# Optimization experiments

Measured on AMD Instinct MI355X. Metric: run time of the kernel, lower is better.

The kernel has to match this reference:

```python
import jax, jax.numpy as jnp
import numpy as np
from jax import lax

B, T, F = 32, 2048, 512
K, D = 1024, 512
CAL = 8
G_MIN, G_MAX = 0.05, 0.75
EPS = 1e-5  # torch LayerNorm default


def setup_inputs() -> dict:
    key = jax.random.key(0)
    ks = jax.random.split(key, 3)
    x = jax.random.normal(ks[0], (B, T, F), dtype=jnp.float32)
    # kaiming_normal_ (fan_in mode, relu gain sqrt(2)) on Linear weights, zero bias
    P_w = jax.random.normal(ks[1], (K, F), dtype=jnp.float32) * np.sqrt(2.0 / F)
    W_w = jax.random.normal(ks[2], (D, K), dtype=jnp.float32) * np.sqrt(2.0 / K)
    return {
        "x": x,
        "P_w": P_w,
        "W_w": W_w,
        "W_b": jnp.zeros((D,), jnp.float32),
        "b": jnp.zeros((D,), jnp.float32),
        "ln_g": jnp.ones((D,), jnp.float32),
        "ln_b": jnp.zeros((D,), jnp.float32),
        "alpha": jnp.float32(0.0),
        "theta1": jnp.float32(0.2),
        "phi1": jnp.float32(0.1),
        "theta2": jnp.float32(0.3),
        "phi2": jnp.float32(0.05),
        "w1": jnp.float32(1.0),
        "w2": jnp.float32(1.0),
        "b_g": jnp.float32(0.0),
    }


def reference(x, P_w, W_w, W_b, b, ln_g, ln_b, alpha, theta1, phi1, theta2, phi2, w1, w2, b_g):
    # --- gate: <Z> of RX(phi) RY(theta) |0> == cos(theta) * cos(phi) ---
    z1 = jnp.cos(theta1) * jnp.cos(phi1)
    z2 = jnp.cos(theta2) * jnp.cos(phi2)
    g = jnp.clip(jax.nn.sigmoid(w1 * z1 + w2 * z2 + b_g), G_MIN, G_MAX)

    # --- calibration scalar (F >= CAL branch) ---
    cal_scalar = x[..., -CAL:].mean(axis=1).mean(axis=1)  # [B]

    # --- per-step linear + bias + alpha*cal, vectorized over (B, T) ---
    proj = jnp.einsum("btf,kf->btk", x, P_w)                    # [B,T,K]
    base = jnp.einsum("btk,dk->btd", proj, W_w) + W_b + b        # [B,T,D]
    base = base + alpha * cal_scalar[:, None, None]

    # --- LayerNorm over last dim (biased variance, as torch) ---
    mu = base.mean(axis=-1, keepdims=True)
    var = jnp.mean(jnp.square(base - mu), axis=-1, keepdims=True)
    base = (base - mu) * lax.rsqrt(var + EPS) * ln_g + ln_b      # [B,T,D]

    # --- scalar-gate EMA recurrence: h_t = (1-g) h_{t-1} + g * base_t ---
    def step(h, bt):
        h = (1.0 - g) * h + g * bt
        return h, None

    h0 = jnp.zeros((x.shape[0], D), dtype=base.dtype)
    h, _ = lax.scan(step, h0, jnp.moveaxis(base, 1, 0))          # scan over T
    return h
```

## Files before the change

### kernel.cpp

```cpp
#include <hip/hip_runtime.h>

#define BB   32
#define TT   2048
#define FF   512
#define KK   1024
#define DD   512
#define NCMAX 512
#define LN_EPS 1e-5f
#define WCUT 1e-12f

typedef __attribute__((ext_vector_type(8))) short bf16x8;
typedef __attribute__((ext_vector_type(4))) float f32x4;

__device__ __forceinline__ float compute_g(const float* th1, const float* ph1,
                                           const float* th2, const float* ph2,
                                           const float* w1, const float* w2,
                                           const float* bg) {
    float z1 = cosf(*th1) * cosf(*ph1);
    float z2 = cosf(*th2) * cosf(*ph2);
    float s  = (*w1) * z1 + (*w2) * z2 + (*bg);
    float sg = 1.0f / (1.0f + expf(-s));
    return fminf(fmaxf(sg, 0.05f), 0.75f);
}

__device__ __forceinline__ ushort f2bf(float x) {
    unsigned u = __float_as_uint(x);
    u += 0x7FFFu + ((u >> 16) & 1u);
    return (ushort)(u >> 16);
}

__global__ __launch_bounds__(256) void weight_merge(
    const float* __restrict__ Pw, const float* __restrict__ Ww,
    ushort* __restrict__ Cbf, float* __restrict__ wj, int* __restrict__ nact,
    float* __restrict__ out,
    const float* th1, const float* ph1, const float* th2, const float* ph2,
    const float* w1p, const float* w2p, const float* bgp) {

    __shared__ __align__(16) ushort As[32 * 16 * 8];
    __shared__ __align__(16) ushort Bs[32 * 16 * 8];
    __shared__ int cnt4[4];

    const int tid = threadIdx.x;

    if (blockIdx.x == 0) {
        const float g   = compute_g(th1, ph1, th2, ph2, w1p, w2p, bgp);
        const float omg = 1.0f - g;
        const float w0  = g * powf(omg, (float)tid);
        const float w1  = g * powf(omg, (float)(tid + 256));
        wj[tid]       = w0;
        wj[tid + 256] = w1;
        const unsigned long long m0 = __ballot(w0 >= WCUT);
        const unsigned long long m1 = __ballot(w1 >= WCUT);
        if ((tid & 63) == 0) cnt4[tid >> 6] = __popcll(m0) + __popcll(m1);
        __syncthreads();
        if (tid == 0) *nact = cnt4[0] + cnt4[1] + cnt4[2] + cnt4[3];
    } else if (blockIdx.x == 1) {
        float4 z = make_float4(0.f, 0.f, 0.f, 0.f);
        #pragma unroll
        for (int i = 0; i < BB * DD / 4 / 256; ++i)
            *(float4*)(out + (size_t)(i * 256 + tid) * 4) = z;
    }

    const int d0 = (blockIdx.x >> 4) * 32;
    const int f0 = (blockIdx.x & 15) * 32;

    const int wave = tid >> 6;
    const int lane = tid & 63;
    const int wm2  = wave >> 1;
    const int wn2  = wave & 1;
    const int lg   = lane >> 4;
    const int ll   = lane & 15;

    const int srow = tid & 31;
    const int so   = tid >> 5;

    const int arow = wm2 * 16 + ll;
    const int brow = wn2 * 16 + ll;

    f32x4 accA = {0.f, 0.f, 0.f, 0.f};
    f32x4 accB = {0.f, 0.f, 0.f, 0.f};

    float a0[8], a1[8], b0[8], b1[8];

#define WM_LOAD(kkv) do {                                                         \
        const float* wr = Ww + (size_t)(d0 + srow) * KK + (kkv);                  \
        *(float4*)&a0[0] = *(const float4*)(wr + so * 8);                         \
        *(float4*)&a0[4] = *(const float4*)(wr + so * 8 + 4);                     \
        *(float4*)&a1[0] = *(const float4*)(wr + (so + 8) * 8);                   \
        *(float4*)&a1[4] = *(const float4*)(wr + (so + 8) * 8 + 4);               \
        const float* pr = Pw + (size_t)(kkv) * FF + f0 + srow;                    \
        _Pragma("unroll")                                                         \
        for (int j = 0; j < 8; ++j) {                                             \
            b0[j] = pr[(size_t)(so * 8 + j) * FF];                                \
            b1[j] = pr[(size_t)((so + 8) * 8 + j) * FF];                          \
        }                                                                         \
    } while (0)

#define WM_STORE() do {                                                           \
        bf16x8 va0, va1, vb0, vb1;                                                \
        _Pragma("unroll")                                                         \
        for (int e = 0; e < 8; ++e) {                                             \
            va0[e] = (short)f2bf(a0[e]); va1[e] = (short)f2bf(a1[e]);             \
            vb0[e] = (short)f2bf(b0[e]); vb1[e] = (short)f2bf(b1[e]);             \
        }                                                                         \
        const int sw = srow & 15;                                                 \
        *(bf16x8*)&As[(srow * 16 + (so ^ sw)) * 8]       = va0;                   \
        *(bf16x8*)&As[(srow * 16 + ((so + 8) ^ sw)) * 8] = va1;                   \
        *(bf16x8*)&Bs[(srow * 16 + (so ^ sw)) * 8]       = vb0;                   \
        *(bf16x8*)&Bs[(srow * 16 + ((so + 8) ^ sw)) * 8] = vb1;                   \
    } while (0)

    WM_LOAD(0);

    for (int kk = 0; kk < KK; kk += 128) {
        WM_STORE();
        __syncthreads();
        if (kk + 128 < KK) WM_LOAD(kk + 128);

        #pragma unroll
        for (int ks = 0; ks < 4; ++ks) {
            const int oct = ks * 4 + lg;
            const bf16x8 af = *(const bf16x8*)&As[(arow * 16 + (oct ^ (arow & 15))) * 8];
            const bf16x8 bf = *(const bf16x8*)&Bs[(brow * 16 + (oct ^ (brow & 15))) * 8];
            if (ks & 1) accB = __builtin_amdgcn_mfma_f32_16x16x32_bf16(af, bf, accB, 0, 0, 0);
            else        accA = __builtin_amdgcn_mfma_f32_16x16x32_bf16(af, bf, accA, 0, 0, 0);
        }
        __syncthreads();
    }
#undef WM_LOAD
#undef WM_STORE

    {
        const f32x4 acc = accA + accB;
        const int fb = f0 + wn2 * 16 + ll;
        const int db = d0 + wm2 * 16 + lg * 4;
        ushort* cp = Cbf + ((size_t)(fb >> 3) * DD) * 8 + (fb & 7);
        #pragma unroll
        for (int j = 0; j < 4; ++j)
            cp[(size_t)(db + j) * 8] = f2bf(acc[j]);
    }
}

__global__ __launch_bounds__(512) void base_ln(
    const float* __restrict__ x, const ushort* __restrict__ Cbf,
    const float* __restrict__ Wb, const float* __restrict__ bvec,
    const float* __restrict__ lng, const float* __restrict__ lnb,
    const float* __restrict__ wj, const int* __restrict__ nact,
    float* __restrict__ out) {

    const int nv = *nact;
    const int cslot = blockIdx.x;
    if (cslot >= nv) return;
    const int rh = blockIdx.y;

    __shared__ __align__(16) ushort xls[16 * 64 * 8];
    __shared__ float redw[8][4][4][2];

    const int tid  = threadIdx.x;
    const int w    = tid >> 6;
    const int lane = tid & 63;
    const int ll   = lane & 15;
    const int lg   = lane >> 4;

    float bias[4], gam[4], bet[4];
    #pragma unroll
    for (int j = 0; j < 4; ++j) {
        const int d = w * 64 + j * 16 + ll;
        bias[j] = Wb[d] + bvec[d];
        gam[j]  = lng[d];
        bet[j]  = lnb[d];
    }

    float hacc[4][4];
    #pragma unroll
    for (int j = 0; j < 4; ++j)
        #pragma unroll
        for (int r = 0; r < 4; ++r) hacc[j][r] = 0.f;

    for (int c = cslot; c < nv; c += 64) {
        const int t = TT - 1 - c;

        #pragma unroll
        for (int i2 = 0; i2 < 2; ++i2) {
            const int i = tid + i2 * 512;
            const int r = i >> 6, o = i & 63;
            const float* src = x + ((size_t)(rh * 16 + r) * TT + t) * FF + o * 8;
            const float4 u0 = *(const float4*)src;
            const float4 u1 = *(const float4*)(src + 4);
            bf16x8 v;
            v[0] = (short)f2bf(u0.x); v[1] = (short)f2bf(u0.y);
            v[2] = (short)f2bf(u0.z); v[3] = (short)f2bf(u0.w);
            v[4] = (short)f2bf(u1.x); v[5] = (short)f2bf(u1.y);
            v[6] = (short)f2bf(u1.z); v[7] = (short)f2bf(u1.w);
            *(bf16x8*)&xls[(r * 64 + (o ^ (r & 7))) * 8] = v;
        }
        __syncthreads();

        f32x4 acc0 = {0.f,0.f,0.f,0.f}, acc1 = {0.f,0.f,0.f,0.f};
        f32x4 acc2 = {0.f,0.f,0.f,0.f}, acc3 = {0.f,0.f,0.f,0.f};

        #pragma unroll 4
        for (int ks = 0; ks < 16; ++ks) {
            const int oct = ks * 4 + lg;
            const bf16x8 af = *(const bf16x8*)&xls[(ll * 64 + (oct ^ (ll & 7))) * 8];
            const ushort* cp = Cbf + ((size_t)oct * DD + w * 64 + ll) * 8;
            const bf16x8 bf0 = *(const bf16x8*)(cp);
            const bf16x8 bf1 = *(const bf16x8*)(cp + 16 * 8);
            const bf16x8 bf2 = *(const bf16x8*)(cp + 32 * 8);
            const bf16x8 bf3 = *(const bf16x8*)(cp + 48 * 8);
            acc0 = __builtin_amdgcn_mfma_f32_16x16x32_bf16(af, bf0, acc0, 0, 0, 0);
            acc1 = __builtin_amdgcn_mfma_f32_16x16x32_bf16(af, bf1, acc1, 0, 0, 0);
            acc2 = __builtin_amdgcn_mfma_f32_16x16x32_bf16(af, bf2, acc2, 0, 0, 0);
            acc3 = __builtin_amdgcn_mfma_f32_16x16x32_bf16(af, bf3, acc3, 0, 0, 0);
        }

        float v[4][4];
        #pragma unroll
        for (int r = 0; r < 4; ++r) {
            v[0][r] = acc0[r] + bias[0];
            v[1][r] = acc1[r] + bias[1];
            v[2][r] = acc2[r] + bias[2];
            v[3][r] = acc3[r] + bias[3];
        }

        float S[4], Q[4];
        #pragma unroll
        for (int r = 0; r < 4; ++r) {
            S[r] = v[0][r] + v[1][r] + v[2][r] + v[3][r];
            Q[r] = v[0][r]*v[0][r] + v[1][r]*v[1][r] + v[2][r]*v[2][r] + v[3][r]*v[3][r];
        }
        #pragma unroll
        for (int off = 8; off >= 1; off >>= 1) {
            #pragma unroll
            for (int r = 0; r < 4; ++r) {
                S[r] += __shfl_xor(S[r], off);
                Q[r] += __shfl_xor(Q[r], off);
            }
        }
        if (ll == 0) {
            #pragma unroll
            for (int r = 0; r < 4; ++r) {
                redw[w][lg][r][0] = S[r];
                redw[w][lg][r][1] = Q[r];
            }
        }
        __syncthreads();

        const float wjc = wj[c];
        #pragma unroll
        for (int r = 0; r < 4; ++r) {
            float SS = 0.f, QQ = 0.f;
            #pragma unroll
            for (int q = 0; q < 8; ++q) {
                SS += redw[q][lg][r][0];
                QQ += redw[q][lg][r][1];
            }
            const float mu   = SS * (1.0f / DD);
            const float rstd = rsqrtf(QQ * (1.0f / DD) - mu * mu + LN_EPS);
            #pragma unroll
            for (int j = 0; j < 4; ++j)
                hacc[j][r] += wjc * ((v[j][r] - mu) * rstd * gam[j] + bet[j]);
        }
        __syncthreads();
    }

    #pragma unroll
    for (int r = 0; r < 4; ++r) {
        const int row = rh * 16 + lg * 4 + r;
        #pragma unroll
        for (int j = 0; j < 4; ++j)
            atomicAdd(out + (size_t)row * DD + w * 64 + j * 16 + ll, hacc[j][r]);
    }
}

extern "C" void kernel_launch(void* const* d_in, const int* in_sizes, int n_in,
                              void* d_out, int out_size, void* d_ws, size_t ws_size,
                              hipStream_t stream) {
    const float* x   = (const float*)d_in[0];
    const float* Pw  = (const float*)d_in[1];
    const float* Ww  = (const float*)d_in[2];
    const float* Wb  = (const float*)d_in[3];
    const float* bv  = (const float*)d_in[4];
    const float* lng = (const float*)d_in[5];
    const float* lnb = (const float*)d_in[6];
    const float* th1 = (const float*)d_in[8];
    const float* ph1 = (const float*)d_in[9];
    const float* th2 = (const float*)d_in[10];
    const float* ph2 = (const float*)d_in[11];
    const float* w1  = (const float*)d_in[12];
    const float* w2  = (const float*)d_in[13];
    const float* bg  = (const float*)d_in[14];

    ushort* Cbf  = (ushort*)d_ws;
    float*  wj   = (float*)((char*)d_ws + (1 << 19));
    int*    nact = (int*)(wj + 512);

    weight_merge<<<256, 256, 0, stream>>>(Pw, Ww, Cbf, wj, nact, (float*)d_out,
                                          th1, ph1, th2, ph2, w1, w2, bg);

    dim3 bgrid(64, 2);
    base_ln<<<bgrid, 512, 0, stream>>>(x, Cbf, Wb, bv, lng, lnb, wj, nact,
                                       (float*)d_out);
}
```

Baseline: 25.94 us.

## Double-buffer weight-merge GEMM staging and coalesce W_w row loads

The weight-merge kernel that forms W_w·P_w now keeps two LDS buffers and two register stages, prefetching two K-tiles ahead, and drops one of the two barriers per iteration. W_w loads are remapped so eight threads read contiguous float4s along a row (rwq/kq8), which coalesces better than the previous per-row pattern. This is meant to hide global load latency in a small prologue GEMM. In exchange it doubles LDS and register use for staging.

Result: faster. 23.18 us (-10.7%).

```diff
diff --git a/kernel.cpp b/kernel.cpp
--- a/kernel.cpp
+++ b/kernel.cpp
@@ -36,8 +36,8 @@
     const float* th1, const float* ph1, const float* th2, const float* ph2,
     const float* w1p, const float* w2p, const float* bgp) {
 
-    __shared__ __align__(16) ushort As[32 * 16 * 8];
-    __shared__ __align__(16) ushort Bs[32 * 16 * 8];
+    __shared__ __align__(16) ushort As[2][32 * 16 * 8];
+    __shared__ __align__(16) ushort Bs[2][32 * 16 * 8];
     __shared__ int cnt4[4];
 
     const int tid = threadIdx.x;
@@ -71,6 +71,8 @@
     const int lg   = lane >> 4;
     const int ll   = lane & 15;
 
+    const int rwq = tid >> 3;
+    const int kq8 = tid & 7;
     const int srow = tid & 31;
     const int so   = tid >> 5;
 
@@ -80,52 +82,60 @@
     f32x4 accA = {0.f, 0.f, 0.f, 0.f};
     f32x4 accB = {0.f, 0.f, 0.f, 0.f};
 
-    float a0[8], a1[8], b0[8], b1[8];
-
-#define WM_LOAD(kkv) do {                                                         \
-        const float* wr = Ww + (size_t)(d0 + srow) * KK + (kkv);                  \
-        *(float4*)&a0[0] = *(const float4*)(wr + so * 8);                         \
-        *(float4*)&a0[4] = *(const float4*)(wr + so * 8 + 4);                     \
-        *(float4*)&a1[0] = *(const float4*)(wr + (so + 8) * 8);                   \
-        *(float4*)&a1[4] = *(const float4*)(wr + (so + 8) * 8 + 4);               \
+    float4 aw[2][4];
+    float  pb0[2][8], pb1[2][8];
+
+#define WM_LOAD(S, kkv) do {                                                      \
+        const float* wr = Ww + (size_t)(d0 + rwq) * KK + (kkv) + kq8 * 4;         \
+        _Pragma("unroll")                                                         \
+        for (int it = 0; it < 4; ++it)                                            \
+            aw[S][it] = *(const float4*)(wr + it * 32);                           \
         const float* pr = Pw + (size_t)(kkv) * FF + f0 + srow;                    \
         _Pragma("unroll")                                                         \
         for (int j = 0; j < 8; ++j) {                                             \
-            b0[j] = pr[(size_t)(so * 8 + j) * FF];                                \
-            b1[j] = pr[(size_t)((so + 8) * 8 + j) * FF];                          \
+            pb0[S][j] = pr[(size_t)(so * 8 + j) * FF];                            \
+            pb1[S][j] = pr[(size_t)((so + 8) * 8 + j) * FF];                      \
         }                                                                         \
     } while (0)
 
-#define WM_STORE() do {                                                           \
-        bf16x8 va0, va1, vb0, vb1;                                                \
+#define WM_STORE(S) do {                                                          \
+        _Pragma("unroll")                                                         \
+        for (int it = 0; it < 4; ++it) {                                          \
+            const int oct  = (kq8 >> 1) + it * 4;                                 \
+            const int half = kq8 & 1;                                             \
+            ushort4 u;                                                            \
+            u.x = f2bf(aw[S][it].x); u.y = f2bf(aw[S][it].y);                     \
+            u.z = f2bf(aw[S][it].z); u.w = f2bf(aw[S][it].w);                     \
+            *(ushort4*)&As[S][(rwq * 16 + (oct ^ (rwq & 15))) * 8 + half * 4] = u;\
+        }                                                                         \
+        bf16x8 vb0, vb1;                                                          \
         _Pragma("unroll")                                                         \
         for (int e = 0; e < 8; ++e) {                                             \
-            va0[e] = (short)f2bf(a0[e]); va1[e] = (short)f2bf(a1[e]);             \
-            vb0[e] = (short)f2bf(b0[e]); vb1[e] = (short)f2bf(b1[e]);             \
+            vb0[e] = (short)f2bf(pb0[S][e]);                                      \
+            vb1[e] = (short)f2bf(pb1[S][e]);                                      \
         }                                                                         \
         const int sw = srow & 15;                                                 \
-        *(bf16x8*)&As[(srow * 16 + (so ^ sw)) * 8]       = va0;                   \
-        *(bf16x8*)&As[(srow * 16 + ((so + 8) ^ sw)) * 8] = va1;                   \
-        *(bf16x8*)&Bs[(srow * 16 + (so ^ sw)) * 8]       = vb0;                   \
-        *(bf16x8*)&Bs[(srow * 16 + ((so + 8) ^ sw)) * 8] = vb1;                   \
+        *(bf16x8*)&Bs[S][(srow * 16 + (so ^ sw)) * 8]       = vb0;                \
+        *(bf16x8*)&Bs[S][(srow * 16 + ((so + 8) ^ sw)) * 8] = vb1;                \
     } while (0)
 
-    WM_LOAD(0);
-
-    for (int kk = 0; kk < KK; kk += 128) {
-        WM_STORE();
-        __syncthreads();
-        if (kk + 128 < KK) WM_LOAD(kk + 128);
-
+    WM_LOAD(0, 0);
+    WM_LOAD(1, 128);
+
+    #pragma unroll
+    for (int k = 0; k < 8; ++k) {
+        const int s = k & 1;
+        WM_STORE(s);
+        if (k + 2 < 8) WM_LOAD(s, (k + 2) * 128);
+        __syncthreads();
         #pragma unroll
         for (int ks = 0; ks < 4; ++ks) {
             const int oct = ks * 4 + lg;
-            const bf16x8 af = *(const bf16x8*)&As[(arow * 16 + (oct ^ (arow & 15))) * 8];
-            const bf16x8 bf = *(const bf16x8*)&Bs[(brow * 16 + (oct ^ (brow & 15))) * 8];
+            const bf16x8 af = *(const bf16x8*)&As[s][(arow * 16 + (oct ^ (arow & 15))) * 8];
+            const bf16x8 bf = *(const bf16x8*)&Bs[s][(brow * 16 + (oct ^ (brow & 15))) * 8];
             if (ks & 1) accB = __builtin_amdgcn_mfma_f32_16x16x32_bf16(af, bf, accB, 0, 0, 0);
             else        accA = __builtin_amdgcn_mfma_f32_16x16x32_bf16(af, bf, accA, 0, 0, 0);
         }
-        __syncthreads();
     }
 #undef WM_LOAD
 #undef WM_STORE
```
